# Kernel tuning notes

Measured on AMD Instinct MI355X. Metric: run time of the kernel, lower is better.

Reference implementation:

```python
import jax, jax.numpy as jnp
import numpy as np

B, S, V, E, H, NL, DFF = 16, 16, 64, 64, 8, 4, 2048
L = S * V
DH = E // H
NUM_GRIDS = 100
POI_DIM = 8
OV_DIM = 8


def setup_inputs() -> dict:
    key = jax.random.key(0)
    ks = jax.random.split(key, 32)
    sc = 0.05
    inp = {}
    inp['features'] = jax.random.normal(ks[0], (B, S, V, 3), jnp.float32)
    inp['overlap_tag'] = jax.random.randint(ks[1], (B, S, V), 0, 3)
    inp['poi_id'] = jax.random.randint(ks[2], (B, S, V), 0, NUM_GRIDS + 1)
    # embedders
    inp['W_raw'] = jax.random.normal(ks[3], (3, E), jnp.float32) * sc
    inp['b_raw'] = jnp.zeros((E,), jnp.float32)
    inp['pos_tab'] = jax.random.normal(ks[4], (S, E), jnp.float32) * sc
    inp['type_tab'] = jax.random.normal(ks[5], (V, E), jnp.float32) * sc
    inp['poi_tab'] = jax.random.normal(ks[6], (NUM_GRIDS + 1, POI_DIM), jnp.float32) * sc
    inp['overlap_tab'] = jax.random.normal(ks[7], (3, OV_DIM), jnp.float32) * sc
    inp['W_comb'] = jax.random.normal(ks[8], (E + OV_DIM + POI_DIM, E), jnp.float32) * sc
    inp['b_comb'] = jnp.zeros((E,), jnp.float32)
    # transformer layers (stacked over NL)
    inp['Wqkv'] = jax.random.normal(ks[9], (NL, E, 3 * E), jnp.float32) * sc
    inp['bqkv'] = jnp.zeros((NL, 3 * E), jnp.float32)
    inp['Wo'] = jax.random.normal(ks[10], (NL, E, E), jnp.float32) * sc
    inp['bo'] = jnp.zeros((NL, E), jnp.float32)
    inp['ln1_s'] = jnp.ones((NL, E), jnp.float32)
    inp['ln1_b'] = jnp.zeros((NL, E), jnp.float32)
    inp['W1'] = jax.random.normal(ks[11], (NL, E, DFF), jnp.float32) * sc
    inp['b1'] = jnp.zeros((NL, DFF), jnp.float32)
    inp['W2'] = jax.random.normal(ks[12], (NL, DFF, E), jnp.float32) * sc
    inp['b2'] = jnp.zeros((NL, E), jnp.float32)
    inp['ln2_s'] = jnp.ones((NL, E), jnp.float32)
    inp['ln2_b'] = jnp.zeros((NL, E), jnp.float32)
    inp['W_head'] = jax.random.normal(ks[13], (E, 3), jnp.float32) * sc
    inp['b_head'] = jnp.zeros((3,), jnp.float32)
    return inp


def _layer_norm(x, s, b):
    m = x.mean(-1, keepdims=True)
    v = ((x - m) ** 2).mean(-1, keepdims=True)
    return (x - m) / jnp.sqrt(v + 1e-5) * s + b


def _forward(features, overlap_tag, poi_id, W_raw, b_raw, pos_tab, type_tab,
             poi_tab, overlap_tab, W_comb, b_comb, Wqkv, bqkv, Wo, bo,
             ln1_s, ln1_b, W1, b1, W2, b2, ln2_s, ln2_b, W_head, b_head):
    # padding_idx=0 rows are zero (as in nn.Embedding(padding_idx=0))
    poi_tab = poi_tab.at[0].set(0.0)
    overlap_tab = overlap_tab.at[0].set(0.0)

    zero_mask = (features.sum(-1) == 0).reshape(B, L)  # [B, L]
    ov_idx = jnp.maximum(overlap_tag, 0)
    poi_idx = jnp.maximum(poi_id, 0)

    feat_e = features @ W_raw + b_raw                    # [B,S,V,E]
    concat = jnp.concatenate([feat_e, overlap_tab[ov_idx], poi_tab[poi_idx]], axis=-1)
    x = (concat @ W_comb + b_comb).reshape(B, L, E)      # [B,L,E]

    t_idx = jnp.repeat(jnp.arange(S), V)                 # [L]
    v_idx = jnp.tile(jnp.arange(V), S)                   # [L]
    struct_mask = (t_idx[:, None] != t_idx[None, :]) & (v_idx[:, None] != v_idx[None, :])
    full_mask = struct_mask[None] | zero_mask[:, None, :] | zero_mask[:, :, None]  # [B,L,L]
    bias = jnp.where(full_mask, -jnp.inf, 0.0)[:, None, :, :]  # [B,1,L,L]

    x = x + pos_tab[t_idx][None] + type_tab[v_idx][None]

    scale = 1.0 / jnp.sqrt(jnp.asarray(DH, x.dtype))
    for l in range(NL):
        qkv = x @ Wqkv[l] + bqkv[l]                      # [B,L,3E]
        q, k, v = jnp.split(qkv, 3, axis=-1)
        q = q.reshape(B, L, H, DH)
        k = k.reshape(B, L, H, DH)
        v = v.reshape(B, L, H, DH)
        scores = jnp.einsum('bqhd,bkhd->bhqk', q, k) * scale + bias
        attn = jax.nn.softmax(scores, axis=-1)
        o = jnp.einsum('bhqk,bkhd->bqhd', attn, v).reshape(B, L, E)
        x = _layer_norm(x + o @ Wo[l] + bo[l], ln1_s[l], ln1_b[l])
        ff = jax.nn.relu(x @ W1[l] + b1[l]) @ W2[l] + b2[l]
        x = _layer_norm(x + ff, ln2_s[l], ln2_b[l])

    last = x.reshape(B, S, V, E)[:, -1]                  # [B,V,E]
    return last @ W_head + b_head                        # [B,V,3]


def reference(features, overlap_tag, poi_id, W_raw, b_raw, pos_tab, type_tab,
              poi_tab, overlap_tab, W_comb, b_comb, Wqkv, bqkv, Wo, bo,
              ln1_s, ln1_b, W1, b1, W2, b2, ln2_s, ln2_b, W_head, b_head):
    return _forward(features, overlap_tag, poi_id, W_raw, b_raw, pos_tab, type_tab,
                    poi_tab, overlap_tab, W_comb, b_comb, Wqkv, bqkv, Wo, bo,
                    ln1_s, ln1_b, W1, b1, W2, b2, ln2_s, ln2_b, W_head, b_head)
```

## Files before the change

### kernel.cpp

```cpp
#include <hip/hip_runtime.h>
#include <math.h>

#define BB 16
#define SS 16
#define VVV 64
#define EE 64
#define HHH 8
#define NLAYER 4
#define DFF_ 2048
#define LL 1024
#define BL 16384
#define PERL 131072

typedef __attribute__((ext_vector_type(8))) _Float16 half8;
typedef __attribute__((ext_vector_type(4))) _Float16 half4v;
typedef __attribute__((ext_vector_type(2))) _Float16 half2v;
typedef __attribute__((ext_vector_type(4))) float f32x4;

#if defined(__has_builtin)
#if __has_builtin(__builtin_amdgcn_fdot2)
#define HAVE_FDOT2 1
#endif
#endif

#define SW64(m, k)  (((m) << 6) + ((((k) >> 3) ^ ((m) & 7)) << 3) + ((k) & 7))


__global__ __launch_bounds__(256) void k_prep(
    const float* __restrict__ W1, const float* __restrict__ W2,
    const float* __restrict__ Wqkv, const float* __restrict__ Wo,
    const float* __restrict__ Wcomb,
    _Float16* __restrict__ w1f, _Float16* __restrict__ w2f,
    _Float16* __restrict__ wqkvf, _Float16* __restrict__ wof,
    _Float16* __restrict__ wcombt)
{
  __shared__ float t[64 * 65];
  int bx = blockIdx.x;
  int cc = threadIdx.x & 63, rr = threadIdx.x >> 6;

  if (bx >= 272) {
    int r0 = (bx - 272) * 64;
#pragma unroll
    for (int i = 0; i < 16; i++) {
      int r = i * 4 + rr;
      if (r0 + r < 80) t[r * 65 + cc] = Wcomb[(size_t)(r0 + r) * 64 + cc];
    }
    __syncthreads();
#pragma unroll
    for (int i = 0; i < 16; i++) {
      int c = i * 4 + rr;
      if (r0 + c < 80) wcombt[(size_t)cc * 80 + r0 + c] = (_Float16)t[c * 65 + cc];
    }
    return;
// ... 25 lines not shown
  __syncthreads();
#pragma unroll
  for (int it = 0; it < 2; it++) {
    int c = threadIdx.x + it * 256;
    int frag = c >> 6, lane = c & 63;
    int m = (frag >> 1) * 16 + (lane & 15);
    int k0 = (frag & 1) * 32 + (lane >> 4) * 8;
    const float* tr = &t[m * 65 + k0];
    half8 h;
#pragma unroll
    for (int j = 0; j < 8; j++) h[j] = (_Float16)tr[j];
    *(half8*)&dst[(size_t)c * 8] = h;
  }
}

__device__ __forceinline__ void qkv_nb(
    const half8 (&af)[2][2], const _Float16* __restrict__ wqkvf,
    const float* __restrict__ bqkv, _Float16* __restrict__ qbuf,
    _Float16* __restrict__ kbuf, _Float16* __restrict__ vbuf,
    int bx, int nb, int wm, int wn, int lane)
{
  int quad = lane >> 4, l15 = lane & 15;
  const _Float16* bt = wqkvf + (size_t)nb * 4096;
  half8 bf[2][2];
#pragma unroll
  for (int nt = 0; nt < 2; nt++)
#pragma unroll
    for (int ks = 0; ks < 2; ks++)
      bf[nt][ks] = *(const half8*)&bt[(size_t)(((wn * 2 + nt) * 2 + ks) * 512) +
                                      lane * 8];
  f32x4 acc[2][2];
#pragma unroll
  for (int mt = 0; mt < 2; mt++)
#pragma unroll
    for (int nt = 0; nt < 2; nt++) {
      float bv = bqkv[nb * 64 + wn * 32 + nt * 16 + l15];
      acc[mt][nt] = (f32x4){bv, bv, bv, bv};
    }
#pragma unroll
  for (int ks = 0; ks < 2; ks++)
#pragma unroll
    for (int mt = 0; mt < 2; mt++)
#pragma unroll
      for (int nt = 0; nt < 2; nt++)
        acc[mt][nt] = __builtin_amdgcn_mfma_f32_16x16x32_f16(
            af[mt][ks], bf[nt][ks], acc[mt][nt], 0, 0, 0);
  _Float16* dst = (nb == 0) ? qbuf : ((nb == 1) ? kbuf : vbuf);
#pragma unroll
  for (int mt = 0; mt < 2; mt++)
#pragma unroll
    for (int nt = 0; nt < 2; nt++) {
      int col = wn * 32 + nt * 16 + l15;
      int h = col >> 3, d = col & 7;
#pragma unroll
      for (int r = 0; r < 4; r++) {
        int row = bx * 64 + wm * 32 + mt * 16 + quad * 4 + r;
        int b = row >> 10, rb = row & 1023;
        dst[((size_t)(b * 8 + h) * 1024 + rb) * 8 + d] = (_Float16)acc[mt][nt][r];
      }
    }
}

__device__ __forceinline__ void ffn_loadw(const _Float16* __restrict__ wt,
                                          half8 (&fr)[4][2], int lane)
{
#pragma unroll
  for (int t = 0; t < 4; t++)
#pragma unroll
    for (int ks = 0; ks < 2; ks++)
      fr[t][ks] = *(const half8*)&wt[(size_t)((t * 2 + ks) * 512) + lane * 8];
}

__device__ __forceinline__ void ffn_chunk(
    const half8 (&a1)[4][2], const half8 (&wb2)[4][2], const half8 (&xb)[2][2],
    _Float16* hw, const float* __restrict__ b1, int g, f32x4 (&acc)[2][4],
    int quad, int l15)
{
// ... 22 lines not shown
      *(half4v*)&hw[SW64(mt * 16 + l15, ht * 16 + quad * 4)] = hp;
    }
  }
#pragma unroll
  for (int ks = 0; ks < 2; ks++)
#pragma unroll
    for (int mt = 0; mt < 2; mt++) {
      half8 a2 = *(const half8*)&hw[SW64(mt * 16 + l15, ks * 32 + quad * 8)];
#pragma unroll
      for (int nt = 0; nt < 4; nt++)
        acc[mt][nt] = __builtin_amdgcn_mfma_f32_16x16x32_f16(a2, wb2[nt][ks],
                                                             acc[mt][nt], 0, 0, 0);
    }
}

__global__ __launch_bounds__(256) void k_embqkv(
    const float* __restrict__ features, const int* __restrict__ ovtag,
    const int* __restrict__ poiid, const float* __restrict__ W_raw,
    const float* __restrict__ b_raw, const float* __restrict__ ov_tab,
    const float* __restrict__ poi_tab, const _Float16* __restrict__ wcombt,
    const float* __restrict__ b_comb, const float* __restrict__ pos_tab,
    const float* __restrict__ type_tab, float* __restrict__ x1,
    float* __restrict__ zm, const _Float16* __restrict__ wqkvf,
    const float* __restrict__ bqkv, _Float16* __restrict__ qbuf,
    _Float16* __restrict__ kbuf, _Float16* __restrict__ vbuf)
{
  constexpr int KP = 104;
  __shared__ _Float16 As[64 * KP];
  __shared__ _Float16 Bs[64 * KP];
  __shared__ _Float16 xs[4096];
  int tid = threadIdx.x;
  int bx = blockIdx.x;
  int m0 = bx * 64;
  int wave = tid >> 6, lane = tid & 63, quad = lane >> 4, l15 = lane & 15;
  int wm = wave >> 1, wn = wave & 1;
  for (int p = tid; p < 1536; p += 256) {
    int r = p / 24, s = p - r * 24; int c = s * 4;
    int row = m0 + r;
    float f0 = features[row * 3 + 0];
    float f1 = features[row * 3 + 1];
    float f2 = features[row * 3 + 2];
    if (s == 0) zm[row] = ((f0 + f1 + f2) == 0.f) ? 1.f : 0.f;
    half4v h;
#pragma unroll
    for (int j = 0; j < 4; j++) {
      int cc = c + j; float v;
      if (cc < 64) {
        v = b_raw[cc] + f0 * W_raw[cc] + f1 * W_raw[64 + cc] + f2 * W_raw[128 + cc];
      } else if (cc < 72) {
        int tt = ovtag[row]; v = (tt <= 0) ? 0.f : ov_tab[tt * 8 + cc - 64];
      } else if (cc < 80) {
        int tt = poiid[row]; v = (tt <= 0) ? 0.f : poi_tab[tt * 8 + cc - 72];
      } else v = 0.f;
      h[j] = (_Float16)v;
    }
    *(half4v*)&As[r * KP + c] = h;
  }
  for (int p = tid; p < 1536; p += 256) {
    int r = p / 24, s = p - r * 24; int c = s * 4;
    half4v h = (half4v){0, 0, 0, 0};
    if (c < 80) h = *(const half4v*)&wcombt[r * 80 + c];
    *(half4v*)&Bs[r * KP + c] = h;
  }
  __syncthreads();
  f32x4 acc[2][2];
#pragma unroll
  for (int mt = 0; mt < 2; mt++)
#pragma unroll
    for (int nt = 0; nt < 2; nt++) {
      float bv = b_comb[wn * 32 + nt * 16 + l15];
      acc[mt][nt] = (f32x4){bv, bv, bv, bv};
    }
#pragma unroll
  for (int ks = 0; ks < 3; ks++) {
    half8 af[2], bf[2];
#pragma unroll
    for (int mt = 0; mt < 2; mt++)
      af[mt] = *(const half8*)&As[(wm * 32 + mt * 16 + l15) * KP + ks * 32 + quad * 8];
#pragma unroll
    for (int nt = 0; nt < 2; nt++)
      bf[nt] = *(const half8*)&Bs[(wn * 32 + nt * 16 + l15) * KP + ks * 32 + quad * 8];
#pragma unroll
    for (int mt = 0; mt < 2; mt++)
#pragma unroll
      for (int nt = 0; nt < 2; nt++)
        acc[mt][nt] = __builtin_amdgcn_mfma_f32_16x16x32_f16(af[mt], bf[nt],
                                                             acc[mt][nt], 0, 0, 0);
  }
#pragma unroll
  for (int mt = 0; mt < 2; mt++)
#pragma unroll
    for (int nt = 0; nt < 2; nt++)
#pragma unroll
      for (int r = 0; r < 4; r++) {
        int lrow = wm * 32 + mt * 16 + quad * 4 + r;
        int row = m0 + lrow;
        int col = wn * 32 + nt * 16 + l15;
        int l = row & (LL - 1);
        float v = acc[mt][nt][r] +
            pos_tab[(l >> 6) * 64 + col] + type_tab[(l & 63) * 64 + col];
        x1[(size_t)row * 64 + col] = v;
        xs[SW64(lrow, col)] = (_Float16)v;
      }
  __syncthreads();
  half8 af[2][2];
#pragma unroll
  for (int mt = 0; mt < 2; mt++)
#pragma unroll
    for (int ks = 0; ks < 2; ks++)
      af[mt][ks] = *(const half8*)&xs[SW64(wm * 32 + mt * 16 + l15,
                                           ks * 32 + quad * 8)];
  for (int nb = 0; nb < 3; nb++)
    qkv_nb(af, wqkvf, bqkv, qbuf, kbuf, vbuf, bx, nb, wm, wn, lane);
}

__global__ __launch_bounds__(256, 2) void k_layerf(
    const _Float16* __restrict__ qin, const _Float16* __restrict__ kin,
    const _Float16* __restrict__ vin, const float* __restrict__ zm,
    const _Float16* __restrict__ wof, const float* __restrict__ bo,
    float* __restrict__ x1,
    const float* __restrict__ ln1_s, const float* __restrict__ ln1_b,
    const _Float16* __restrict__ w1f, const _Float16* __restrict__ w2f,
    const float* __restrict__ b1, const float* __restrict__ b2,
    const float* __restrict__ ln2_s, const float* __restrict__ ln2_b,
    const _Float16* __restrict__ wqkvf, const float* __restrict__ bqkv,
    _Float16* __restrict__ qout, _Float16* __restrict__ kout,
    _Float16* __restrict__ vout, int doqkv,
    const float* __restrict__ Wh, const float* __restrict__ bh,
    float* __restrict__ out)
{
  __shared__ float ots[32 * 68];
  __shared__ float ots2[32 * 68];
  __shared__ __align__(16) _Float16 xs[2048];
  __shared__ float x2f[2048];
  __shared__ __align__(16) _Float16 hs[4][2048];
  __shared__ __align__(16) _Float16 os[2048];
  __shared__ float zsh[1024];
  int tid = threadIdx.x;
  int bx = blockIdx.x;
  int r0 = bx * 32;
  int wave = tid >> 6, lane = tid & 63;
  int quad = lane >> 4, l15 = lane & 15;
  int grp = wave >> 1, wn = wave & 1;
  int b = r0 >> 10;

  for (int p = tid; p < 1024; p += 256)
    zsh[p] = (zm[b * LL + p] != 0.f) ? -20000.f : 0.f;

  half8 obf[2][2];
#pragma unroll
  for (int nt = 0; nt < 2; nt++)
#pragma unroll
    for (int ks = 0; ks < 2; ks++)
      obf[nt][ks] = *(const half8*)&wof[(size_t)(((wn * 2 + nt) * 2 + ks) * 512) +
                                        lane * 8];
  float x1pre[8];
#pragma unroll
  for (int i = 0; i < 8; i++)
    x1pre[i] = x1[(size_t)(r0 + wave * 8 + i) * 64 + lane];
  float ln1sv = ln1_s[lane], ln1bv = ln1_b[lane];
  float ln2sv = ln2_s[lane], ln2bv = ln2_b[lane];
  float fb2 = b2[lane];
  __syncthreads();

  {
    int lr = tid & 31, hh = tid >> 5;
    int rb = (r0 & 1023) + lr;
    int tq = rb >> 6, vq = rb & 63;
    const _Float16* kb = kin + (size_t)(b * 8 + hh) * 8192;
    const _Float16* vb = vin + (size_t)(b * 8 + hh) * 8192;
    half8 qh = *(const half8*)&qin[(size_t)(b * 8 + hh) * 8192 + (size_t)rb * 8];
    const float scale = 0.3535533905932738f;
    float m = -10000.f, lsum = 0.f;
    float acc[8] = {0.f, 0.f, 0.f, 0.f, 0.f, 0.f, 0.f, 0.f};
    bool zmq = (zsh[rb] < -1.f);

    auto attend = [&](int k) {
      half8 kk = *(const half8*)&kb[(size_t)k * 8];
      half8 vv = *(const half8*)&vb[(size_t)k * 8];
      float s = 0.f;
#ifdef HAVE_FDOT2
#pragma unroll
      for (int j = 0; j < 4; j++) {
        half2v qa = (half2v){qh[2 * j], qh[2 * j + 1]};
        half2v ka = (half2v){kk[2 * j], kk[2 * j + 1]};
        s = __builtin_amdgcn_fdot2(qa, ka, s, false);
      }
#else
#pragma unroll
      for (int j = 0; j < 8; j++) s += (float)qh[j] * (float)kk[j];
#endif
      s = s * scale + zsh[k];
      float nm = fmaxf(m, s);
      float r = __expf(m - nm);
      float p = __expf(s - nm);
      lsum = lsum * r + p;
#pragma unroll
      for (int d = 0; d < 8; d++) acc[d] = acc[d] * r + p * (float)vv[d];
      m = nm;
    };

    if (!zmq) {
      for (int vv2 = 0; vv2 < 64; vv2++) attend(tq * 64 + vv2);
      for (int tt = 0; tt < 16; tt++) {
        if (tt == tq) continue;
        attend(tt * 64 + vq);
      }
    }
    float inv = (lsum > 0.f) ? 1.f / lsum : 0.f;
    half8 o;
#pragma unroll
    for (int d = 0; d < 8; d++) o[d] = (_Float16)(acc[d] * inv);
    *(half8*)&os[SW64(lr, hh * 8)] = o;
  }
  __syncthreads();

  {
    half8 af[2];
#pragma unroll
    for (int ks = 0; ks < 2; ks++)
      af[ks] = *(const half8*)&os[SW64(grp * 16 + l15, ks * 32 + quad * 8)];
    f32x4 acc[2];
#pragma unroll
    for (int nt = 0; nt < 2; nt++) {
      float bv = bo[wn * 32 + nt * 16 + l15];
      acc[nt] = (f32x4){bv, bv, bv, bv};
    }
#pragma unroll
    for (int ks = 0; ks < 2; ks++)
#pragma unroll
      for (int nt = 0; nt < 2; nt++)
        acc[nt] = __builtin_amdgcn_mfma_f32_16x16x32_f16(af[ks], obf[nt][ks],
                                                         acc[nt], 0, 0, 0);
#pragma unroll
    for (int nt = 0; nt < 2; nt++)
#pragma unroll
      for (int r = 0; r < 4; r++)
        ots[(grp * 16 + quad * 4 + r) * 68 + wn * 32 + nt * 16 + l15] = acc[nt][r];
  }
  half8 a1x[4][2], b2x[4][2], a1y[4][2], b2y[4][2];
  ffn_loadw(w1f + (size_t)wave * 4096, a1x, lane);
  ffn_loadw(w2f + (size_t)wave * 4096, b2x, lane);
  __syncthreads();
  for (int i = 0; i < 8; i++) {
    int row = wave * 8 + i;
    float val = ots[row * 68 + lane] + x1pre[i];
    float sum = val;
#pragma unroll
    for (int o = 32; o > 0; o >>= 1) sum += __shfl_xor(sum, o);
    float mean = sum * (1.f / 64.f);
    float d = val - mean;
    float sq = d * d;
#pragma unroll
    for (int o = 32; o > 0; o >>= 1) sq += __shfl_xor(sq, o);
    float xv = d * rsqrtf(sq * (1.f / 64.f) + 1e-5f) * ln1sv + ln1bv;
    x2f[row * 64 + lane] = xv;
    xs[SW64(row, lane)] = (_Float16)xv;
  }
  __syncthreads();

  half8 xb[2][2];
#pragma unroll
  for (int mt = 0; mt < 2; mt++)
#pragma unroll
    for (int ks = 0; ks < 2; ks++)
      xb[mt][ks] = *(const half8*)&xs[SW64(mt * 16 + l15, ks * 32 + quad * 8)];
  f32x4 facc[2][4];
#pragma unroll
  for (int mt = 0; mt < 2; mt++)
#pragma unroll
    for (int nt = 0; nt < 4; nt++) facc[mt][nt] = (f32x4){0.f, 0.f, 0.f, 0.f};
  _Float16* hw = &hs[wave][0];
  for (int ii = 0; ii < 4; ii++) {
    int gy = ii * 8 + 4 + wave;
    ffn_loadw(w1f + (size_t)gy * 4096, a1y, lane);
    ffn_loadw(w2f + (size_t)gy * 4096, b2y, lane);
    ffn_chunk(a1x, b2x, xb, hw, b1, ii * 8 + wave, facc, quad, l15);
    if (ii < 3) {
      ffn_loadw(w1f + (size_t)(gy + 4) * 4096, a1x, lane);
      ffn_loadw(w2f + (size_t)(gy + 4) * 4096, b2x, lane);
    }
    ffn_chunk(a1y, b2y, xb, hw, b1, gy, facc, quad, l15);
  }
  if (wave < 2) {
    float* dst = (wave == 0) ? ots : ots2;
#pragma unroll
    for (int mt = 0; mt < 2; mt++)
#pragma unroll
      for (int nt = 0; nt < 4; nt++)
#pragma unroll
        for (int r = 0; r < 4; r++)
          dst[(mt * 16 + quad * 4 + r) * 68 + nt * 16 + l15] = facc[mt][nt][r];
  }
  __syncthreads();
  if (wave >= 2) {
    float* dst = (wave == 2) ? ots : ots2;
#pragma unroll
    for (int mt = 0; mt < 2; mt++)
#pragma unroll
      for (int nt = 0; nt < 4; nt++)
#pragma unroll
        for (int r = 0; r < 4; r++)
          dst[(mt * 16 + quad * 4 + r) * 68 + nt * 16 + l15] += facc[mt][nt][r];
  }
  __syncthreads();
  for (int i = 0; i < 8; i++) {
    int row = wave * 8 + i;
    size_t off = (size_t)(r0 + row) * 64 + lane;
    float val = ots[row * 68 + lane] + ots2[row * 68 + lane] + fb2 +
                x2f[row * 64 + lane];
    float sum = val;
#pragma unroll
    for (int o = 32; o > 0; o >>= 1) sum += __shfl_xor(sum, o);
    float mean = sum * (1.f / 64.f);
    float d = val - mean;
    float sq = d * d;
#pragma unroll
    for (int o = 32; o > 0; o >>= 1) sq += __shfl_xor(sq, o);
    float xv = d * rsqrtf(sq * (1.f / 64.f) + 1e-5f) * ln2sv + ln2bv;
    x1[off] = xv;
    x2f[row * 64 + lane] = xv;
    xs[SW64(row, lane)] = (_Float16)xv;
  }
  if (!doqkv) {
    __syncthreads();
    if ((bx & 31) >= 30 && tid < 96) {
      int bb2 = bx >> 5;
      int i = tid / 3, j = tid - i * 3;
      int vglob = (bx & 1) * 32 + i;
      float a = bh[j];
      for (int e = 0; e < 64; e++)
        a += x2f[i * 64 + e] * Wh[e * 3 + j];
      out[((size_t)(bb2 * 64 + vglob)) * 3 + j] = a;
    }
    return;
  }
  __syncthreads();
  half8 af[2][2];
#pragma unroll
  for (int mt = 0; mt < 2; mt++)
#pragma unroll
    for (int ks = 0; ks < 2; ks++)
      af[mt][ks] = *(const half8*)&xs[SW64(mt * 16 + l15, ks * 32 + quad * 8)];
  for (int nb = 0; nb < 3; nb++) {
    const _Float16* bt = wqkvf + (size_t)nb * 4096;
    half8 bf[2];
#pragma unroll
    for (int ks = 0; ks < 2; ks++)
      bf[ks] = *(const half8*)&bt[(size_t)((wave * 2 + ks) * 512) + lane * 8];
    f32x4 qacc[2];
#pragma unroll
    for (int mt = 0; mt < 2; mt++) {
      float bv = bqkv[nb * 64 + wave * 16 + l15];
      qacc[mt] = (f32x4){bv, bv, bv, bv};
    }
#pragma unroll
    for (int ks = 0; ks < 2; ks++)
#pragma unroll
      for (int mt = 0; mt < 2; mt++)
        qacc[mt] = __builtin_amdgcn_mfma_f32_16x16x32_f16(af[mt][ks], bf[ks],
                                                          qacc[mt], 0, 0, 0);
    _Float16* dst = (nb == 0) ? qout : ((nb == 1) ? kout : vout);
    int col = wave * 16 + l15;
    int h2 = col >> 3, d2 = col & 7;
#pragma unroll
    for (int mt = 0; mt < 2; mt++)
#pragma unroll
      for (int r = 0; r < 4; r++) {
        int row = r0 + mt * 16 + quad * 4 + r;
        int rbq = row & 1023;
        dst[((size_t)(b * 8 + h2) * 1024 + rbq) * 8 + d2] = (_Float16)qacc[mt][r];
      }
  }
}

extern "C" void kernel_launch(void* const* d_in, const int* in_sizes, int n_in,
                              void* d_out, int out_size, void* d_ws, size_t ws_size,
                              hipStream_t stream) {
  const float* features = (const float*)d_in[0];
  const int*   ovtag    = (const int*)d_in[1];
  const int*   poiid    = (const int*)d_in[2];
  const float* W_raw    = (const float*)d_in[3];
  const float* b_raw    = (const float*)d_in[4];
  const float* pos_tab  = (const float*)d_in[5];
  const float* type_tab = (const float*)d_in[6];
  const float* poi_tab  = (const float*)d_in[7];
  const float* ov_tab   = (const float*)d_in[8];
// ... 4 lines not shown
  const float* Wo       = (const float*)d_in[13];
  const float* bo       = (const float*)d_in[14];
  const float* ln1_s    = (const float*)d_in[15];
  const float* ln1_b    = (const float*)d_in[16];
  const float* W1       = (const float*)d_in[17];
  const float* b1       = (const float*)d_in[18];
  const float* W2       = (const float*)d_in[19];
  const float* b2       = (const float*)d_in[20];
  const float* ln2_s    = (const float*)d_in[21];
  const float* ln2_b    = (const float*)d_in[22];
  const float* W_head   = (const float*)d_in[23];
  const float* b_head   = (const float*)d_in[24];
  float* out = (float*)d_out;
  float* ws  = (float*)d_ws;

  float* zm  = ws;
  float* x1  = zm + BL;
  _Float16* qbA = (_Float16*)(x1 + (size_t)BL * 64);
  _Float16* kbA = qbA + (size_t)BL * 64;
  _Float16* vbA = kbA + (size_t)BL * 64;
  _Float16* qbB = vbA + (size_t)BL * 64;
  _Float16* kbB = qbB + (size_t)BL * 64;
  _Float16* vbB = kbB + (size_t)BL * 64;
  _Float16* wcombt = vbB + (size_t)BL * 64;
  _Float16* w1f    = wcombt + 5120;
  _Float16* w2f    = w1f + (size_t)NLAYER * PERL;
  _Float16* wqkvf  = w2f + (size_t)NLAYER * PERL;
  _Float16* wof    = wqkvf + (size_t)NLAYER * 3 * 4096;

  k_prep<<<274, 256, 0, stream>>>(W1, W2, Wqkv, Wo, W_comb,
                                  w1f, w2f, wqkvf, wof, wcombt);
  k_embqkv<<<256, 256, 0, stream>>>(features, ovtag, poiid, W_raw, b_raw,
                                    ov_tab, poi_tab, wcombt, b_comb,
                                    pos_tab, type_tab, x1, zm,
                                    wqkvf, bqkv, qbA, kbA, vbA);
  for (int l = 0; l < NLAYER; l++) {
    const _Float16* qin = (l & 1) ? qbB : qbA;
    const _Float16* kin = (l & 1) ? kbB : kbA;
    const _Float16* vin = (l & 1) ? vbB : vbA;
    _Float16* qout = (l & 1) ? qbA : qbB;
    _Float16* kout = (l & 1) ? kbA : kbB;
    _Float16* vout = (l & 1) ? vbA : vbB;
    int doqkv = (l < NLAYER - 1);
    k_layerf<<<512, 256, 0, stream>>>(
        qin, kin, vin, zm,
        wof + (size_t)l * 4096, bo + l * EE, x1,
        ln1_s + l * EE, ln1_b + l * EE,
        w1f + (size_t)l * PERL, w2f + (size_t)l * PERL,
        b1 + l * DFF_, b2 + l * EE,
        ln2_s + l * EE, ln2_b + l * EE,
        wqkvf + (size_t)(l + 1 < NLAYER ? l + 1 : 0) * 3 * 4096,
        bqkv + (l + 1 < NLAYER ? l + 1 : 0) * 192,
        qout, kout, vout, doqkv, W_head, b_head, out);
  }
}
```

Baseline: 291.4 us.

## Fuse embedding and all layers into one persistent kernel with grid barriers

Replaces the embed+QKV kernel and the four per-layer launches with a single persistent kernel of 512 blocks. A software grid barrier built on atomics separates the layers. Each block keeps its residual rows and Q in shared memory across layers, so the x1 and Q global round-trips go away and only K/V are exchanged through global memory. This removes launch gaps and tail effects between layers. In exchange it relies on all 512 blocks being co-resident (2 per CU on 256 CUs), or the barrier deadlocks, and it adds barrier spin overhead.

```diff
diff --git a/kernel.cpp b/kernel.cpp
--- a/kernel.cpp
+++ b/kernel.cpp
@@ -11,6 +11,7 @@
 #define LL 1024
 #define BL 16384
 #define PERL 131072
+#define NBLK 512
 
 typedef __attribute__((ext_vector_type(8))) _Float16 half8;
 typedef __attribute__((ext_vector_type(4))) _Float16 half4v;
@@ -25,6 +26,28 @@
 
 #define SW64(m, k)  (((m) << 6) + ((((k) >> 3) ^ ((m) & 7)) << 3) + ((k) & 7))
 
+__device__ __forceinline__ void gsync(unsigned int* bar, int tid) {
+  __syncthreads();
+  __threadfence();
+  if (tid == 0) {
+    unsigned int g = __hip_atomic_load(&bar[32], __ATOMIC_RELAXED,
+                                       __HIP_MEMORY_SCOPE_AGENT);
+    unsigned int prev = __hip_atomic_fetch_add(&bar[0], 1u, __ATOMIC_ACQ_REL,
+                                               __HIP_MEMORY_SCOPE_AGENT);
+    if (prev == (unsigned int)(NBLK - 1)) {
+      __hip_atomic_store(&bar[0], 0u, __ATOMIC_RELAXED,
+                         __HIP_MEMORY_SCOPE_AGENT);
+      __hip_atomic_fetch_add(&bar[32], 1u, __ATOMIC_RELEASE,
+                             __HIP_MEMORY_SCOPE_AGENT);
+    } else {
+      while (__hip_atomic_load(&bar[32], __ATOMIC_ACQUIRE,
+                               __HIP_MEMORY_SCOPE_AGENT) == g)
+        __builtin_amdgcn_s_sleep(2);
+    }
+  }
+  __syncthreads();
+  __threadfence();
+}
 
 __global__ __launch_bounds__(256) void k_prep(
     const float* __restrict__ W1, const float* __restrict__ W2,
@@ -32,11 +55,13 @@
     const float* __restrict__ Wcomb,
     _Float16* __restrict__ w1f, _Float16* __restrict__ w2f,
     _Float16* __restrict__ wqkvf, _Float16* __restrict__ wof,
-    _Float16* __restrict__ wcombt)
+    _Float16* __restrict__ wcombt, unsigned int* __restrict__ bar)
 {
   __shared__ float t[64 * 65];
   int bx = blockIdx.x;
   int cc = threadIdx.x & 63, rr = threadIdx.x >> 6;
+
+  if (bx == 0 && threadIdx.x < 64) bar[threadIdx.x] = 0;
 
   if (bx >= 272) {
     int r0 = (bx - 272) * 64;
@@ -92,53 +117,6 @@
   }
 }
 
-__device__ __forceinline__ void qkv_nb(
-    const half8 (&af)[2][2], const _Float16* __restrict__ wqkvf,
-    const float* __restrict__ bqkv, _Float16* __restrict__ qbuf,
-    _Float16* __restrict__ kbuf, _Float16* __restrict__ vbuf,
-    int bx, int nb, int wm, int wn, int lane)
-{
-  int quad = lane >> 4, l15 = lane & 15;
-  const _Float16* bt = wqkvf + (size_t)nb * 4096;
-  half8 bf[2][2];
-#pragma unroll
-  for (int nt = 0; nt < 2; nt++)
-#pragma unroll
-    for (int ks = 0; ks < 2; ks++)
-      bf[nt][ks] = *(const half8*)&bt[(size_t)(((wn * 2 + nt) * 2 + ks) * 512) +
-                                      lane * 8];
-  f32x4 acc[2][2];
-#pragma unroll
-  for (int mt = 0; mt < 2; mt++)
-#pragma unroll
-    for (int nt = 0; nt < 2; nt++) {
-      float bv = bqkv[nb * 64 + wn * 32 + nt * 16 + l15];
-      acc[mt][nt] = (f32x4){bv, bv, bv, bv};
-    }
-#pragma unroll
-  for (int ks = 0; ks < 2; ks++)
-#pragma unroll
-    for (int mt = 0; mt < 2; mt++)
-#pragma unroll
-      for (int nt = 0; nt < 2; nt++)
-        acc[mt][nt] = __builtin_amdgcn_mfma_f32_16x16x32_f16(
-            af[mt][ks], bf[nt][ks], acc[mt][nt], 0, 0, 0);
-  _Float16* dst = (nb == 0) ? qbuf : ((nb == 1) ? kbuf : vbuf);
-#pragma unroll
-  for (int mt = 0; mt < 2; mt++)
-#pragma unroll
-    for (int nt = 0; nt < 2; nt++) {
-      int col = wn * 32 + nt * 16 + l15;
-      int h = col >> 3, d = col & 7;
-#pragma unroll
-      for (int r = 0; r < 4; r++) {
-        int row = bx * 64 + wm * 32 + mt * 16 + quad * 4 + r;
-        int b = row >> 10, rb = row & 1023;
-        dst[((size_t)(b * 8 + h) * 1024 + rb) * 8 + d] = (_Float16)acc[mt][nt][r];
-      }
-    }
-}
-
 __device__ __forceinline__ void ffn_loadw(const _Float16* __restrict__ wt,
                                           half8 (&fr)[4][2], int lane)
 {
@@ -191,363 +169,361 @@
     }
 }
 
-__global__ __launch_bounds__(256) void k_embqkv(
-    const float* __restrict__ features, const int* __restrict__ ovtag,
-    const int* __restrict__ poiid, const float* __restrict__ W_raw,
-    const float* __restrict__ b_raw, const float* __restrict__ ov_tab,
-    const float* __restrict__ poi_tab, const _Float16* __restrict__ wcombt,
-    const float* __restrict__ b_comb, const float* __restrict__ pos_tab,
-    const float* __restrict__ type_tab, float* __restrict__ x1,
-    float* __restrict__ zm, const _Float16* __restrict__ wqkvf,
-    const float* __restrict__ bqkv, _Float16* __restrict__ qbuf,
-    _Float16* __restrict__ kbuf, _Float16* __restrict__ vbuf)
+__device__ __forceinline__ void qkv32(
+    const _Float16* xs, _Float16* qkvt,
+    const _Float16* __restrict__ wq, const float* __restrict__ bq,
+    _Float16* __restrict__ kout, _Float16* __restrict__ vout,
+    int b, int rb0, int wave, int lane, int tid)
 {
-  constexpr int KP = 104;
-  __shared__ _Float16 As[64 * KP];
-  __shared__ _Float16 Bs[64 * KP];
-  __shared__ _Float16 xs[4096];
+  int quad = lane >> 4, l15 = lane & 15;
+  half8 af[2][2];
+#pragma unroll
+  for (int mt = 0; mt < 2; mt++)
+#pragma unroll
+    for (int ks = 0; ks < 2; ks++)
+      af[mt][ks] = *(const half8*)&xs[SW64(mt * 16 + l15, ks * 32 + quad * 8)];
+#pragma unroll
+  for (int nb = 0; nb < 3; nb++) {
+    const _Float16* bt = wq + (size_t)nb * 4096;
+    half8 bf[2];
+#pragma unroll
+    for (int ks = 0; ks < 2; ks++)
+      bf[ks] = *(const half8*)&bt[(size_t)((wave * 2 + ks) * 512) + lane * 8];
+    f32x4 qacc[2];
+#pragma unroll
+    for (int mt = 0; mt < 2; mt++) {
+      float bv = bq[nb * 64 + wave * 16 + l15];
+      qacc[mt] = (f32x4){bv, bv, bv, bv};
+    }
+#pragma unroll
+    for (int ks = 0; ks < 2; ks++)
+#pragma unroll
+      for (int mt = 0; mt < 2; mt++)
+        qacc[mt] = __builtin_amdgcn_mfma_f32_16x16x32_f16(af[mt][ks], bf[ks],
+                                                          qacc[mt], 0, 0, 0);
+#pragma unroll
+    for (int mt = 0; mt < 2; mt++)
+#pragma unroll
+      for (int r = 0; r < 4; r++)
+        qkvt[(mt * 16 + quad * 4 + r) * 200 + nb * 64 + wave * 16 + l15] =
+            (_Float16)qacc[mt][r];
+  }
+  __syncthreads();
+  int h = tid >> 5, lr = tid & 31;
+  size_t rb = (size_t)rb0 + lr;
+  half8 kv = *(const half8*)&qkvt[lr * 200 + 64 + h * 8];
+  half8 vv = *(const half8*)&qkvt[lr * 200 + 128 + h * 8];
+  *(half8*)&kout[((size_t)(b * 8 + h) * 1024 + rb) * 8] = kv;
+  *(half8*)&vout[((size_t)(b * 8 + h) * 1024 + rb) * 8] = vv;
+}
+
+struct PArgs {
+  const float* features; const int* ovtag; const int* poiid;
+  const float* W_raw; const float* b_raw;
+  const float* ov_tab; const float* poi_tab;
+  const _Float16* wcombt; const float* b_comb;
+  const float* pos_tab; const float* type_tab;
+  float* zm;
+  const _Float16* wqkvf; const float* bqkv;
+  const _Float16* wof; const float* bo;
+  const float* ln1_s; const float* ln1_b;
+  const _Float16* w1f; const _Float16* w2f;
+  const float* b1; const float* b2;
+  const float* ln2_s; const float* ln2_b;
+  const float* Wh; const float* bh; float* out;
+  _Float16* kA; _Float16* vA; _Float16* kB; _Float16* vB;
+  unsigned int* bar;
+};
+
+__global__ __launch_bounds__(256, 2) void k_persist(PArgs P)
+{
+  __shared__ __align__(16) char smem[54272];
+  float*    ots  = (float*)smem;
+  float*    ots2 = (float*)(smem + 8704);
+  _Float16* xs   = (_Float16*)(smem + 17408);
+  float*    x2f  = (float*)(smem + 21504);
+  _Float16* hs   = (_Float16*)(smem + 29696);
+  _Float16* os   = (_Float16*)(smem + 46080);
+  float*    zsh  = (float*)(smem + 50176);
+  _Float16* As   = (_Float16*)smem;
+  _Float16* Bs   = hs;
+  _Float16* qkvt = hs;
+
   int tid = threadIdx.x;
   int bx = blockIdx.x;
-  int m0 = bx * 64;
-  int wave = tid >> 6, lane = tid & 63, quad = lane >> 4, l15 = lane & 15;
-  int wm = wave >> 1, wn = wave & 1;
-  for (int p = tid; p < 1536; p += 256) {
-    int r = p / 24, s = p - r * 24; int c = s * 4;
-    int row = m0 + r;
-    float f0 = features[row * 3 + 0];
-    float f1 = features[row * 3 + 1];
-    float f2 = features[row * 3 + 2];
-    if (s == 0) zm[row] = ((f0 + f1 + f2) == 0.f) ? 1.f : 0.f;
+  int r0 = bx * 32;
+  int rb0 = r0 & 1023;
+  int b = r0 >> 10;
+  int wave = tid >> 6, lane = tid & 63;
+  int quad = lane >> 4, l15 = lane & 15;
+
+  for (int p = tid; p < 832; p += 256) {
+    int r = p / 26, s = p - r * 26; int c = s * 4;
+    int row = r0 + r;
+    float f0 = P.features[row * 3 + 0];
+    float f1 = P.features[row * 3 + 1];
+    float f2 = P.features[row * 3 + 2];
+    if (s == 0) P.zm[row] = ((f0 + f1 + f2) == 0.f) ? 1.f : 0.f;
     half4v h;
 #pragma unroll
     for (int j = 0; j < 4; j++) {
       int cc = c + j; float v;
       if (cc < 64) {
-        v = b_raw[cc] + f0 * W_raw[cc] + f1 * W_raw[64 + cc] + f2 * W_raw[128 + cc];
+        v = P.b_raw[cc] + f0 * P.W_raw[cc] + f1 * P.W_raw[64 + cc] +
+            f2 * P.W_raw[128 + cc];
       } else if (cc < 72) {
-        int tt = ovtag[row]; v = (tt <= 0) ? 0.f : ov_tab[tt * 8 + cc - 64];
+        int tt = P.ovtag[row]; v = (tt <= 0) ? 0.f : P.ov_tab[tt * 8 + cc - 64];
       } else if (cc < 80) {
-        int tt = poiid[row]; v = (tt <= 0) ? 0.f : poi_tab[tt * 8 + cc - 72];
+        int tt = P.poiid[row]; v = (tt <= 0) ? 0.f : P.poi_tab[tt * 8 + cc - 72];
       } else v = 0.f;
       h[j] = (_Float16)v;
     }
-    *(half4v*)&As[r * KP + c] = h;
-  }
-  for (int p = tid; p < 1536; p += 256) {
-    int r = p / 24, s = p - r * 24; int c = s * 4;
+    *(half4v*)&As[r * 104 + c] = h;
+  }
+  for (int p = tid; p < 1664; p += 256) {
+    int r = p / 26, s = p - r * 26; int c = s * 4;
     half4v h = (half4v){0, 0, 0, 0};
-    if (c < 80) h = *(const half4v*)&wcombt[r * 80 + c];
-    *(half4v*)&Bs[r * KP + c] = h;
+    if (c < 80) h = *(const half4v*)&P.wcombt[r * 80 + c];
+    *(half4v*)&Bs[r * 104 + c] = h;
   }
   __syncthreads();
-  f32x4 acc[2][2];
-#pragma unroll
-  for (int mt = 0; mt < 2; mt++)
+  {
+    int wm = wave >> 1, wn = wave & 1;
+    f32x4 acc[2];
 #pragma unroll
     for (int nt = 0; nt < 2; nt++) {
-      float bv = b_comb[wn * 32 + nt * 16 + l15];
-      acc[mt][nt] = (f32x4){bv, bv, bv, bv};
-    }
-#pragma unroll
-  for (int ks = 0; ks < 3; ks++) {
-    half8 af[2], bf[2];
-#pragma unroll
-    for (int mt = 0; mt < 2; mt++)
-      af[mt] = *(const half8*)&As[(wm * 32 + mt * 16 + l15) * KP + ks * 32 + quad * 8];
+      float bv = P.b_comb[wn * 32 + nt * 16 + l15];
+      acc[nt] = (f32x4){bv, bv, bv, bv};
+    }
+#pragma unroll
+    for (int ks = 0; ks < 3; ks++) {
+      half8 af = *(const half8*)&As[(wm * 16 + l15) * 104 + ks * 32 + quad * 8];
+      half8 bf[2];
+#pragma unroll
+      for (int nt = 0; nt < 2; nt++)
+        bf[nt] = *(const half8*)&Bs[(wn * 32 + nt * 16 + l15) * 104 + ks * 32 +
+                                    quad * 8];
+#pragma unroll
+      for (int nt = 0; nt < 2; nt++)
+        acc[nt] = __builtin_amdgcn_mfma_f32_16x16x32_f16(af, bf[nt], acc[nt],
+                                                         0, 0, 0);
+    }
+    __syncthreads();
 #pragma unroll
     for (int nt = 0; nt < 2; nt++)
-      bf[nt] = *(const half8*)&Bs[(wn * 32 + nt * 16 + l15) * KP + ks * 32 + quad * 8];
-#pragma unroll
-    for (int mt = 0; mt < 2; mt++)
-#pragma unroll
-      for (int nt = 0; nt < 2; nt++)
-        acc[mt][nt] = __builtin_amdgcn_mfma_f32_16x16x32_f16(af[mt], bf[nt],
-                                                             acc[mt][nt], 0, 0, 0);
-  }
-#pragma unroll
-  for (int mt = 0; mt < 2; mt++)
-#pragma unroll
-    for (int nt = 0; nt < 2; nt++)
 #pragma unroll
       for (int r = 0; r < 4; r++) {
-        int lrow = wm * 32 + mt * 16 + quad * 4 + r;
-        int row = m0 + lrow;
+        int lrow = wm * 16 + quad * 4 + r;
+        int row = r0 + lrow;
         int col = wn * 32 + nt * 16 + l15;
         int l = row & (LL - 1);
-        float v = acc[mt][nt][r] +
-            pos_tab[(l >> 6) * 64 + col] + type_tab[(l & 63) * 64 + col];
-        x1[(size_t)row * 64 + col] = v;
+        float v = acc[nt][r] +
+            P.pos_tab[(l >> 6) * 64 + col] + P.type_tab[(l & 63) * 64 + col];
+        x2f[lrow * 64 + col] = v;
         xs[SW64(lrow, col)] = (_Float16)v;
       }
+  }
   __syncthreads();
-  half8 af[2][2];
-#pragma unroll
-  for (int mt = 0; mt < 2; mt++)
-#pragma unroll
-    for (int ks = 0; ks < 2; ks++)
-      af[mt][ks] = *(const half8*)&xs[SW64(wm * 32 + mt * 16 + l15,
-                                           ks * 32 + quad * 8)];
-  for (int nb = 0; nb < 3; nb++)
-    qkv_nb(af, wqkvf, bqkv, qbuf, kbuf, vbuf, bx, nb, wm, wn, lane);
-}
-
-__global__ __launch_bounds__(256, 2) void k_layerf(
-    const _Float16* __restrict__ qin, const _Float16* __restrict__ kin,
-    const _Float16* __restrict__ vin, const float* __restrict__ zm,
-    const _Float16* __restrict__ wof, const float* __restrict__ bo,
-    float* __restrict__ x1,
-    const float* __restrict__ ln1_s, const float* __restrict__ ln1_b,
-    const _Float16* __restrict__ w1f, const _Float16* __restrict__ w2f,
-    const float* __restrict__ b1, const float* __restrict__ b2,
-    const float* __restrict__ ln2_s, const float* __restrict__ ln2_b,
-    const _Float16* __restrict__ wqkvf, const float* __restrict__ bqkv,
-    _Float16* __restrict__ qout, _Float16* __restrict__ kout,
-    _Float16* __restrict__ vout, int doqkv,
-    const float* __restrict__ Wh, const float* __restrict__ bh,
-    float* __restrict__ out)
-{
-  __shared__ float ots[32 * 68];
-  __shared__ float ots2[32 * 68];
-  __shared__ __align__(16) _Float16 xs[2048];
-  __shared__ float x2f[2048];
-  __shared__ __align__(16) _Float16 hs[4][2048];
-  __shared__ __align__(16) _Float16 os[2048];
-  __shared__ float zsh[1024];
-  int tid = threadIdx.x;
-  int bx = blockIdx.x;
-  int r0 = bx * 32;
-  int wave = tid >> 6, lane = tid & 63;
-  int quad = lane >> 4, l15 = lane & 15;
-  int grp = wave >> 1, wn = wave & 1;
-  int b = r0 >> 10;
-
-  for (int p = tid; p < 1024; p += 256)
-    zsh[p] = (zm[b * LL + p] != 0.f) ? -20000.f : 0.f;
-
-  half8 obf[2][2];
-#pragma unroll
-  for (int nt = 0; nt < 2; nt++)
-#pragma unroll
-    for (int ks = 0; ks < 2; ks++)
-      obf[nt][ks] = *(const half8*)&wof[(size_t)(((wn * 2 + nt) * 2 + ks) * 512) +
-                                        lane * 8];
-  float x1pre[8];
-#pragma unroll
-  for (int i = 0; i < 8; i++)
-    x1pre[i] = x1[(size_t)(r0 + wave * 8 + i) * 64 + lane];
-  float ln1sv = ln1_s[lane], ln1bv = ln1_b[lane];
-  float ln2sv = ln2_s[lane], ln2bv = ln2_b[lane];
-  float fb2 = b2[lane];
-  __syncthreads();
-
-  {
-    int lr = tid & 31, hh = tid >> 5;
-    int rb = (r0 & 1023) + lr;
-    int tq = rb >> 6, vq = rb & 63;
-    const _Float16* kb = kin + (size_t)(b * 8 + hh) * 8192;
-    const _Float16* vb = vin + (size_t)(b * 8 + hh) * 8192;
-    half8 qh = *(const half8*)&qin[(size_t)(b * 8 + hh) * 8192 + (size_t)rb * 8];
-    const float scale = 0.3535533905932738f;
-    float m = -10000.f, lsum = 0.f;
-    float acc[8] = {0.f, 0.f, 0.f, 0.f, 0.f, 0.f, 0.f, 0.f};
-    bool zmq = (zsh[rb] < -1.f);
-
-    auto attend = [&](int k) {
-      half8 kk = *(const half8*)&kb[(size_t)k * 8];
-      half8 vv = *(const half8*)&vb[(size_t)k * 8];
-      float s = 0.f;
+  qkv32(xs, qkvt, P.wqkvf, P.bqkv, P.kA, P.vA, b, rb0, wave, lane, tid);
+
+  for (int l = 0; l < NLAYER; ++l) {
+    gsync(P.bar, tid);
+    const _Float16* kin = (l & 1) ? P.kB : P.kA;
+    const _Float16* vin = (l & 1) ? P.vB : P.vA;
+    if (l == 0) {
+      for (int p = tid; p < 1024; p += 256)
+        zsh[p] = (P.zm[b * LL + p] != 0.f) ? -20000.f : 0.f;
+      __syncthreads();
+    }
+    const _Float16* wof_l = P.wof + (size_t)l * 4096;
+    int grp = wave >> 1, wn = wave & 1;
+    half8 obf[2][2];
+#pragma unroll
+    for (int nt = 0; nt < 2; nt++)
+#pragma unroll
+      for (int ks = 0; ks < 2; ks++)
+        obf[nt][ks] = *(const half8*)&wof_l[(size_t)(((wn * 2 + nt) * 2 + ks) * 512)
+                                            + lane * 8];
+    float ln1sv = P.ln1_s[l * 64 + lane], ln1bv = P.ln1_b[l * 64 + lane];
+    float ln2sv = P.ln2_s[l * 64 + lane], ln2bv = P.ln2_b[l * 64 + lane];
+    float fb2 = P.b2[l * 64 + lane];
+
+    {
+      int lr = tid & 31, hh = tid >> 5;
+      int rb = rb0 + lr;
+      int tq = rb >> 6, vq = rb & 63;
+      const _Float16* kb = kin + (size_t)(b * 8 + hh) * 8192;
+      const _Float16* vb = vin + (size_t)(b * 8 + hh) * 8192;
+      half8 qh = *(const half8*)&qkvt[lr * 200 + hh * 8];
+      const float scale = 0.3535533905932738f;
+      float m = -10000.f, lsum = 0.f;
+      float acc[8] = {0.f, 0.f, 0.f, 0.f, 0.f, 0.f, 0.f, 0.f};
+      bool zmq = (zsh[rb] < -1.f);
+
+      auto attend = [&](int k) {
+        half8 kk = *(const half8*)&kb[(size_t)k * 8];
+        half8 vv = *(const half8*)&vb[(size_t)k * 8];
+        float s = 0.f;
 #ifdef HAVE_FDOT2
 #pragma unroll
-      for (int j = 0; j < 4; j++) {
-        half2v qa = (half2v){qh[2 * j], qh[2 * j + 1]};
-        half2v ka = (half2v){kk[2 * j], kk[2 * j + 1]};
-        s = __builtin_amdgcn_fdot2(qa, ka, s, false);
+        for (int j = 0; j < 4; j++) {
+          half2v qa = (half2v){qh[2 * j], qh[2 * j + 1]};
+          half2v ka = (half2v){kk[2 * j], kk[2 * j + 1]};
+          s = __builtin_amdgcn_fdot2(qa, ka, s, false);
+        }
+#else
+#pragma unroll
+        for (int j = 0; j < 8; j++) s += (float)qh[j] * (float)kk[j];
+#endif
+        s = s * scale + zsh[k];
+        float nm = fmaxf(m, s);
+        float r = __expf(m - nm);
+        float p = __expf(s - nm);
+        lsum = lsum * r + p;
+#pragma unroll
+        for (int d = 0; d < 8; d++) acc[d] = acc[d] * r + p * (float)vv[d];
+        m = nm;
+      };
+
+      if (!zmq) {
+        for (int vv2 = 0; vv2 < 64; vv2++) attend(tq * 64 + vv2);
+        for (int tt = 0; tt < 16; tt++) {
+          if (tt == tq) continue;
+          attend(tt * 64 + vq);
+        }
       }
-#else
-#pragma unroll
-      for (int j = 0; j < 8; j++) s += (float)qh[j] * (float)kk[j];
-#endif
-      s = s * scale + zsh[k];
-      float nm = fmaxf(m, s);
-      float r = __expf(m - nm);
-      float p = __expf(s - nm);
-      lsum = lsum * r + p;
-#pragma unroll
-      for (int d = 0; d < 8; d++) acc[d] = acc[d] * r + p * (float)vv[d];
-      m = nm;
-    };
-
-    if (!zmq) {
-      for (int vv2 = 0; vv2 < 64; vv2++) attend(tq * 64 + vv2);
-      for (int tt = 0; tt < 16; tt++) {
-        if (tt == tq) continue;
-        attend(tt * 64 + vq);
+      float inv = (lsum > 0.f) ? 1.f / lsum : 0.f;
+      half8 o;
+#pragma unroll
+      for (int d = 0; d < 8; d++) o[d] = (_Float16)(acc[d] * inv);
+      *(half8*)&os[SW64(lr, hh * 8)] = o;
+    }
+    __syncthreads();
+
+    {
+      half8 af[2];
+#pragma unroll
+      for (int ks = 0; ks < 2; ks++)
+        af[ks] = *(const half8*)&os[SW64(grp * 16 + l15, ks * 32 + quad * 8)];
+      f32x4 acc[2];
+#pragma unroll
+      for (int nt = 0; nt < 2; nt++) {
+        float bv = P.bo[l * 64 + wn * 32 + nt * 16 + l15];
+        acc[nt] = (f32x4){bv, bv, bv, bv};
       }
-    }
-    float inv = (lsum > 0.f) ? 1.f / lsum : 0.f;
-    half8 o;
-#pragma unroll
-    for (int d = 0; d < 8; d++) o[d] = (_Float16)(acc[d] * inv);
-    *(half8*)&os[SW64(lr, hh * 8)] = o;
-  }
-  __syncthreads();
-
-  {
-    half8 af[2];
-#pragma unroll
-    for (int ks = 0; ks < 2; ks++)
-      af[ks] = *(const half8*)&os[SW64(grp * 16 + l15, ks * 32 + quad * 8)];
-    f32x4 acc[2];
-#pragma unroll
-    for (int nt = 0; nt < 2; nt++) {
-      float bv = bo[wn * 32 + nt * 16 + l15];
-      acc[nt] = (f32x4){bv, bv, bv, bv};
-    }
-#pragma unroll
-    for (int ks = 0; ks < 2; ks++)
+#pragma unroll
+      for (int ks = 0; ks < 2; ks++)
+#pragma unroll
+        for (int nt = 0; nt < 2; nt++)
+          acc[nt] = __builtin_amdgcn_mfma_f32_16x16x32_f16(af[ks], obf[nt][ks],
+                                                           acc[nt], 0, 0, 0);
 #pragma unroll
       for (int nt = 0; nt < 2; nt++)
-        acc[nt] = __builtin_amdgcn_mfma_f32_16x16x32_f16(af[ks], obf[nt][ks],
-                                                         acc[nt], 0, 0, 0);
-#pragma unroll
-    for (int nt = 0; nt < 2; nt++)
-#pragma unroll
-      for (int r = 0; r < 4; r++)
-        ots[(grp * 16 + quad * 4 + r) * 68 + wn * 32 + nt * 16 + l15] = acc[nt][r];
-  }
-  half8 a1x[4][2], b2x[4][2], a1y[4][2], b2y[4][2];
-  ffn_loadw(w1f + (size_t)wave * 4096, a1x, lane);
-  ffn_loadw(w2f + (size_t)wave * 4096, b2x, lane);
-  __syncthreads();
-  for (int i = 0; i < 8; i++) {
-    int row = wave * 8 + i;
-    float val = ots[row * 68 + lane] + x1pre[i];
-    float sum = val;
-#pragma unroll
-    for (int o = 32; o > 0; o >>= 1) sum += __shfl_xor(sum, o);
-    float mean = sum * (1.f / 64.f);
-    float d = val - mean;
-    float sq = d * d;
-#pragma unroll
-    for (int o = 32; o > 0; o >>= 1) sq += __shfl_xor(sq, o);
-    float xv = d * rsqrtf(sq * (1.f / 64.f) + 1e-5f) * ln1sv + ln1bv;
-    x2f[row * 64 + lane] = xv;
-    xs[SW64(row, lane)] = (_Float16)xv;
-  }
-  __syncthreads();
-
-  half8 xb[2][2];
-#pragma unroll
-  for (int mt = 0; mt < 2; mt++)
-#pragma unroll
-    for (int ks = 0; ks < 2; ks++)
-      xb[mt][ks] = *(const half8*)&xs[SW64(mt * 16 + l15, ks * 32 + quad * 8)];
-  f32x4 facc[2][4];
-#pragma unroll
-  for (int mt = 0; mt < 2; mt++)
-#pragma unroll
-    for (int nt = 0; nt < 4; nt++) facc[mt][nt] = (f32x4){0.f, 0.f, 0.f, 0.f};
-  _Float16* hw = &hs[wave][0];
-  for (int ii = 0; ii < 4; ii++) {
-    int gy = ii * 8 + 4 + wave;
-    ffn_loadw(w1f + (size_t)gy * 4096, a1y, lane);
-    ffn_loadw(w2f + (size_t)gy * 4096, b2y, lane);
-    ffn_chunk(a1x, b2x, xb, hw, b1, ii * 8 + wave, facc, quad, l15);
-    if (ii < 3) {
-      ffn_loadw(w1f + (size_t)(gy + 4) * 4096, a1x, lane);
-      ffn_loadw(w2f + (size_t)(gy + 4) * 4096, b2x, lane);
-    }
-    ffn_chunk(a1y, b2y, xb, hw, b1, gy, facc, quad, l15);
-  }
-  if (wave < 2) {
-    float* dst = (wave == 0) ? ots : ots2;
+#pragma unroll
+        for (int r = 0; r < 4; r++)
+          ots[(grp * 16 + quad * 4 + r) * 68 + wn * 32 + nt * 16 + l15] =
+              acc[nt][r];
+    }
+    half8 a1x[4][2], b2x[4][2], a1y[4][2], b2y[4][2];
+    const _Float16* w1l = P.w1f + (size_t)l * PERL;
+    const _Float16* w2l = P.w2f + (size_t)l * PERL;
+    ffn_loadw(w1l + (size_t)wave * 4096, a1x, lane);
+    ffn_loadw(w2l + (size_t)wave * 4096, b2x, lane);
+    __syncthreads();
+    for (int i = 0; i < 8; i++) {
+      int row = wave * 8 + i;
+      float val = ots[row * 68 + lane] + x2f[row * 64 + lane];
+      float sum = val;
+#pragma unroll
+      for (int o = 32; o > 0; o >>= 1) sum += __shfl_xor(sum, o);
+      float mean = sum * (1.f / 64.f);
+      float d = val - mean;
+      float sq = d * d;
+#pragma unroll
+      for (int o = 32; o > 0; o >>= 1) sq += __shfl_xor(sq, o);
+      float xv = d * rsqrtf(sq * (1.f / 64.f) + 1e-5f) * ln1sv + ln1bv;
+      x2f[row * 64 + lane] = xv;
+      xs[SW64(row, lane)] = (_Float16)xv;
+    }
+    __syncthreads();
+
+    half8 xb[2][2];
 #pragma unroll
     for (int mt = 0; mt < 2; mt++)
 #pragma unroll
-      for (int nt = 0; nt < 4; nt++)
-#pragma unroll
-        for (int r = 0; r < 4; r++)
-          dst[(mt * 16 + quad * 4 + r) * 68 + nt * 16 + l15] = facc[mt][nt][r];
-  }
-  __syncthreads();
-  if (wave >= 2) {
-    float* dst = (wave == 2) ? ots : ots2;
+      for (int ks = 0; ks < 2; ks++)
+        xb[mt][ks] = *(const half8*)&xs[SW64(mt * 16 + l15, ks * 32 + quad * 8)];
+    f32x4 facc[2][4];
 #pragma unroll
     for (int mt = 0; mt < 2; mt++)
 #pragma unroll
-      for (int nt = 0; nt < 4; nt++)
-#pragma unroll
-        for (int r = 0; r < 4; r++)
-          dst[(mt * 16 + quad * 4 + r) * 68 + nt * 16 + l15] += facc[mt][nt][r];
-  }
-  __syncthreads();
-  for (int i = 0; i < 8; i++) {
-    int row = wave * 8 + i;
-    size_t off = (size_t)(r0 + row) * 64 + lane;
-    float val = ots[row * 68 + lane] + ots2[row * 68 + lane] + fb2 +
-                x2f[row * 64 + lane];
-    float sum = val;
-#pragma unroll
-    for (int o = 32; o > 0; o >>= 1) sum += __shfl_xor(sum, o);
-    float mean = sum * (1.f / 64.f);
-    float d = val - mean;
-    float sq = d * d;
-#pragma unroll
-    for (int o = 32; o > 0; o >>= 1) sq += __shfl_xor(sq, o);
-    float xv = d * rsqrtf(sq * (1.f / 64.f) + 1e-5f) * ln2sv + ln2bv;
-    x1[off] = xv;
-    x2f[row * 64 + lane] = xv;
-    xs[SW64(row, lane)] = (_Float16)xv;
-  }
-  if (!doqkv) {
-    __syncthreads();
-    if ((bx & 31) >= 30 && tid < 96) {
-      int bb2 = bx >> 5;
-      int i = tid / 3, j = tid - i * 3;
-      int vglob = (bx & 1) * 32 + i;
-      float a = bh[j];
-      for (int e = 0; e < 64; e++)
-        a += x2f[i * 64 + e] * Wh[e * 3 + j];
-      out[((size_t)(bb2 * 64 + vglob)) * 3 + j] = a;
-    }
-    return;
-  }
-  __syncthreads();
-  half8 af[2][2];
-#pragma unroll
-  for (int mt = 0; mt < 2; mt++)
-#pragma unroll
-    for (int ks = 0; ks < 2; ks++)
-      af[mt][ks] = *(const half8*)&xs[SW64(mt * 16 + l15, ks * 32 + quad * 8)];
-  for (int nb = 0; nb < 3; nb++) {
-    const _Float16* bt = wqkvf + (size_t)nb * 4096;
-    half8 bf[2];
-#pragma unroll
-    for (int ks = 0; ks < 2; ks++)
-      bf[ks] = *(const half8*)&bt[(size_t)((wave * 2 + ks) * 512) + lane * 8];
-    f32x4 qacc[2];
-#pragma unroll
-    for (int mt = 0; mt < 2; mt++) {
-      float bv = bqkv[nb * 64 + wave * 16 + l15];
-      qacc[mt] = (f32x4){bv, bv, bv, bv};
-    }
-#pragma unroll
-    for (int ks = 0; ks < 2; ks++)
+      for (int nt = 0; nt < 4; nt++) facc[mt][nt] = (f32x4){0.f, 0.f, 0.f, 0.f};
+    _Float16* hw = &hs[wave * 2048];
+    const float* b1l = P.b1 + (size_t)l * DFF_;
+    for (int ii = 0; ii < 4; ii++) {
+      int gy = ii * 8 + 4 + wave;
+      ffn_loadw(w1l + (size_t)gy * 4096, a1y, lane);
+      ffn_loadw(w2l + (size_t)gy * 4096, b2y, lane);
+      ffn_chunk(a1x, b2x, xb, hw, b1l, ii * 8 + wave, facc, quad, l15);
+      if (ii < 3) {
+        ffn_loadw(w1l + (size_t)(gy + 4) * 4096, a1x, lane);
+        ffn_loadw(w2l + (size_t)(gy + 4) * 4096, b2x, lane);
+      }
+      ffn_chunk(a1y, b2y, xb, hw, b1l, gy, facc, quad, l15);
+    }
+    if (wave < 2) {
+      float* dst = (wave == 0) ? ots : ots2;
 #pragma unroll
       for (int mt = 0; mt < 2; mt++)
-        qacc[mt] = __builtin_amdgcn_mfma_f32_16x16x32_f16(af[mt][ks], bf[ks],
-                                                          qacc[mt], 0, 0, 0);
-    _Float16* dst = (nb == 0) ? qout : ((nb == 1) ? kout : vout);
-    int col = wave * 16 + l15;
-    int h2 = col >> 3, d2 = col & 7;
-#pragma unroll
-    for (int mt = 0; mt < 2; mt++)
-#pragma unroll
-      for (int r = 0; r < 4; r++) {
-        int row = r0 + mt * 16 + quad * 4 + r;
-        int rbq = row & 1023;
-        dst[((size_t)(b * 8 + h2) * 1024 + rbq) * 8 + d2] = (_Float16)qacc[mt][r];
+#pragma unroll
+        for (int nt = 0; nt < 4; nt++)
+#pragma unroll
+          for (int r = 0; r < 4; r++)
+            dst[(mt * 16 + quad * 4 + r) * 68 + nt * 16 + l15] = facc[mt][nt][r];
+    }
+    __syncthreads();
+    if (wave >= 2) {
+      float* dst = (wave == 2) ? ots : ots2;
+#pragma unroll
+      for (int mt = 0; mt < 2; mt++)
+#pragma unroll
+        for (int nt = 0; nt < 4; nt++)
+#pragma unroll
+          for (int r = 0; r < 4; r++)
+            dst[(mt * 16 + quad * 4 + r) * 68 + nt * 16 + l15] += facc[mt][nt][r];
+    }
+    __syncthreads();
+    for (int i = 0; i < 8; i++) {
+      int row = wave * 8 + i;
+      float val = ots[row * 68 + lane] + ots2[row * 68 + lane] + fb2 +
+                  x2f[row * 64 + lane];
+      float sum = val;
+#pragma unroll
+      for (int o = 32; o > 0; o >>= 1) sum += __shfl_xor(sum, o);
+      float mean = sum * (1.f / 64.f);
+      float d = val - mean;
+      float sq = d * d;
+#pragma unroll
+      for (int o = 32; o > 0; o >>= 1) sq += __shfl_xor(sq, o);
+      float xv = d * rsqrtf(sq * (1.f / 64.f) + 1e-5f) * ln2sv + ln2bv;
+      x2f[row * 64 + lane] = xv;
+      xs[SW64(row, lane)] = (_Float16)xv;
+    }
+    __syncthreads();
+    if (l < NLAYER - 1) {
+      qkv32(xs, qkvt, P.wqkvf + (size_t)(l + 1) * 3 * 4096, P.bqkv + (l + 1) * 192,
+            (l & 1) ? P.kA : P.kB, (l & 1) ? P.vA : P.vB, b, rb0, wave, lane, tid);
+    } else {
+      if ((bx & 31) >= 30 && tid < 96) {
+        int bb2 = bx >> 5;
+        int i = tid / 3, j = tid - i * 3;
+        int vglob = (bx & 1) * 32 + i;
+        float a = P.bh[j];
+        for (int e = 0; e < 64; e++)
+          a += x2f[i * 64 + e] * P.Wh[e * 3 + j];
+        P.out[((size_t)(bb2 * 64 + vglob)) * 3 + j] = a;
       }
+    }
   }
 }
 
@@ -582,43 +558,37 @@
   float* out = (float*)d_out;
   float* ws  = (float*)d_ws;
 
-  float* zm  = ws;
-  float* x1  = zm + BL;
-  _Float16* qbA = (_Float16*)(x1 + (size_t)BL * 64);
-  _Float16* kbA = qbA + (size_t)BL * 64;
-  _Float16* vbA = kbA + (size_t)BL * 64;
-  _Float16* qbB = vbA + (size_t)BL * 64;
-  _Float16* kbB = qbB + (size_t)BL * 64;
-  _Float16* vbB = kbB + (size_t)BL * 64;
-  _Float16* wcombt = vbB + (size_t)BL * 64;
+  float* zm = ws;
+  _Float16* kA = (_Float16*)(zm + BL);
+  _Float16* vA = kA + (size_t)BL * 64;
+  _Float16* kB = vA + (size_t)BL * 64;
+  _Float16* vB = kB + (size_t)BL * 64;
+  _Float16* wcombt = vB + (size_t)BL * 64;
   _Float16* w1f    = wcombt + 5120;
   _Float16* w2f    = w1f + (size_t)NLAYER * PERL;
   _Float16* wqkvf  = w2f + (size_t)NLAYER * PERL;
   _Float16* wof    = wqkvf + (size_t)NLAYER * 3 * 4096;
+  unsigned int* bar = (unsigned int*)(wof + (size_t)NLAYER * 4096);
 
   k_prep<<<274, 256, 0, stream>>>(W1, W2, Wqkv, Wo, W_comb,
-                                  w1f, w2f, wqkvf, wof, wcombt);
-  k_embqkv<<<256, 256, 0, stream>>>(features, ovtag, poiid, W_raw, b_raw,
-                                    ov_tab, poi_tab, wcombt, b_comb,
-                                    pos_tab, type_tab, x1, zm,
-                                    wqkvf, bqkv, qbA, kbA, vbA);
-  for (int l = 0; l < NLAYER; l++) {
-    const _Float16* qin = (l & 1) ? qbB : qbA;
-    const _Float16* kin = (l & 1) ? kbB : kbA;
-    const _Float16* vin = (l & 1) ? vbB : vbA;
-    _Float16* qout = (l & 1) ? qbA : qbB;
-    _Float16* kout = (l & 1) ? kbA : kbB;
-    _Float16* vout = (l & 1) ? vbA : vbB;
-    int doqkv = (l < NLAYER - 1);
-    k_layerf<<<512, 256, 0, stream>>>(
-        qin, kin, vin, zm,
-        wof + (size_t)l * 4096, bo + l * EE, x1,
-        ln1_s + l * EE, ln1_b + l * EE,
-        w1f + (size_t)l * PERL, w2f + (size_t)l * PERL,
-        b1 + l * DFF_, b2 + l * EE,
-        ln2_s + l * EE, ln2_b + l * EE,
-        wqkvf + (size_t)(l + 1 < NLAYER ? l + 1 : 0) * 3 * 4096,
-        bqkv + (l + 1 < NLAYER ? l + 1 : 0) * 192,
-        qout, kout, vout, doqkv, W_head, b_head, out);
-  }
-}
+                                  w1f, w2f, wqkvf, wof, wcombt, bar);
+
+  PArgs pa;
+  pa.features = features; pa.ovtag = ovtag; pa.poiid = poiid;
+  pa.W_raw = W_raw; pa.b_raw = b_raw;
+  pa.ov_tab = ov_tab; pa.poi_tab = poi_tab;
+  pa.wcombt = wcombt; pa.b_comb = b_comb;
+  pa.pos_tab = pos_tab; pa.type_tab = type_tab;
+  pa.zm = zm;
+  pa.wqkvf = wqkvf; pa.bqkv = bqkv;
+  pa.wof = wof; pa.bo = bo;
+  pa.ln1_s = ln1_s; pa.ln1_b = ln1_b;
+  pa.w1f = w1f; pa.w2f = w2f;
+  pa.b1 = b1; pa.b2 = b2;
+  pa.ln2_s = ln2_s; pa.ln2_b = ln2_b;
+  pa.Wh = W_head; pa.bh = b_head; pa.out = out;
+  pa.kA = kA; pa.vA = vA; pa.kB = kB; pa.vB = vB;
+  pa.bar = bar;
+
+  k_persist<<<NBLK, 256, 0, stream>>>(pa);
+}
```

Measured after the change: 760.4 us. 161% more time.
